# Kernel tuning notes

Measured on AMD Instinct MI355X. Metric: run time of the kernel, lower is better.

## Reference

```python
import jax, jax.numpy as jnp
import numpy as np

NUM_HEADS = 16
NUM_KV_HEADS = 4
ROPE_THETA = 10000.0


def apply_rope(x, position_ids, theta):
    # x: [B, S, h, d]; position_ids: [B, S]
    d = x.shape[-1]
    freqs = 1.0 / theta ** (jnp.arange(0, d, 2, dtype=jnp.float32) / d)  # [d/2]
    angles = position_ids.astype(jnp.float32)[..., None] * freqs          # [B, S, d/2]
    cos = jnp.cos(angles)[:, :, None, :]                                  # [B, S, 1, d/2]
    sin = jnp.sin(angles)[:, :, None, :]
    xr = x.astype(jnp.float32).reshape(*x.shape[:-1], d // 2, 2)
    x0, x1 = xr[..., 0], xr[..., 1]
    o0 = x0 * cos - x1 * sin
    o1 = x0 * sin + x1 * cos
    out = jnp.stack((o0, o1), axis=-1).reshape(*x.shape)
    return out.astype(x.dtype)


def setup_inputs() -> dict:
    key = jax.random.key(0)
    k0, k1, k2, k3, k4 = jax.random.split(key, 5)
    B, S, H = 1, 2048, 2048
    Hkv = H // (NUM_HEADS // NUM_KV_HEADS)  # 512
    init_scale = 0.02 / np.sqrt(H)
    return {
        "hidden_states": jax.random.normal(k0, (B, S, H), jnp.float32),
        "attention_mask": jnp.ones((B, S), jnp.int32),
        "segment_ids": jnp.zeros((B, S), jnp.int32),
        "position_ids": jnp.broadcast_to(jnp.arange(S, dtype=jnp.int32)[None], (B, S)),
        "Wq": jax.random.normal(k1, (H, H), jnp.float32) * init_scale,
        "Wk": jax.random.normal(k2, (H, Hkv), jnp.float32) * init_scale,
        "Wv": jax.random.normal(k3, (H, Hkv), jnp.float32) * init_scale,
        "Wo": jax.random.normal(k4, (H, H), jnp.float32) * init_scale,
    }


def reference(hidden_states, attention_mask, segment_ids, position_ids, Wq, Wk, Wv, Wo):
    B, S, H = hidden_states.shape
    nh, nkv = NUM_HEADS, NUM_KV_HEADS
    g = nh // nkv
    hd = H // nh

    xq = (hidden_states @ Wq).reshape(B, S, nh, hd)
    xk = (hidden_states @ Wk).reshape(B, S, nkv, hd)
    xv = (hidden_states @ Wv).reshape(B, S, nkv, hd)
    # GQA repeat: 'b s (h d) -> b s (h g) d' == repeat each kv head g times contiguously
    xk = jnp.repeat(xk, g, axis=2)  # [B, S, nh, hd]
    xv = jnp.repeat(xv, g, axis=2)

    xq = apply_rope(xq, position_ids, ROPE_THETA)
    xk = apply_rope(xk, position_ids, ROPE_THETA)

    # masks: causal AND padding AND segment
    causal = jnp.tril(jnp.ones((S, S), dtype=bool))[None, None]            # [1,1,S,S]
    pad = (attention_mask > 0)[:, None, None, :]                            # [B,1,1,S]
    seg = (segment_ids[:, :, None] == segment_ids[:, None, :])[:, None]     # [B,1,S,S]
    mask = causal & pad & seg                                               # [B,1,S,S]

    scale = 1.0 / np.sqrt(hd)
    logits = jnp.einsum("bqhd,bkhd->bhqk", xq.astype(jnp.float32), xk.astype(jnp.float32)) * scale
    logits = jnp.where(mask, logits, jnp.finfo(jnp.float32).min)
    probs = jax.nn.softmax(logits, axis=-1).astype(xv.dtype)
    attn = jnp.einsum("bhqk,bkhd->bqhd", probs, xv)                         # [B,S,nh,hd]

    out = attn.reshape(B, S, H) @ Wo
    return out
```

## Files before the change

kernel.cpp:

```cpp
#include <hip/hip_runtime.h>
#include <hip/hip_bf16.h>
#include <stdint.h>
#include <math.h>

#define SS 2048
#define HH 2048
#define NH 16
#define NKV 4
#define HD 128
#define HKV 512
#define NQKV 3072

typedef __bf16 bf16x8 __attribute__((ext_vector_type(8)));
typedef float f32x4 __attribute__((ext_vector_type(4)));

static_assert(sizeof(bf16x8) == 16, "bf16x8 must be 16B");

__device__ __forceinline__ void async_ld16(const void* gp, void* lp) {
  __builtin_amdgcn_global_load_lds(
      (const __attribute__((address_space(1))) unsigned int*)(uintptr_t)gp,
      (__attribute__((address_space(3))) unsigned int*)(uintptr_t)lp,
      16, 0, 0);
}

__device__ __forceinline__ unsigned short f2bu(float f) {
  __hip_bfloat16 b = __float2bfloat16(f);
  return *reinterpret_cast<unsigned short*>(&b);
}

__global__ __launch_bounds__(256) void k_prep1(
    const float* __restrict__ X, const float* __restrict__ Wq, const float* __restrict__ Wk,
    const float* __restrict__ Wv, const float* __restrict__ Wo,
    const int* __restrict__ amv, const int* __restrict__ seg, int* __restrict__ kseg,
    __hip_bfloat16* __restrict__ Xb, __hip_bfloat16* __restrict__ WqT,
    __hip_bfloat16* __restrict__ WkT, __hip_bfloat16* __restrict__ WvT,
    __hip_bfloat16* __restrict__ WoT) {
  __shared__ float tile[32][33];
  int b = blockIdx.x;
  if (b < 4096) {
    int i = b * 256 + threadIdx.y * 32 + threadIdx.x;
    float4 v = ((const float4*)X)[i];
    ushort4 o;
    o.x = f2bu(v.x); o.y = f2bu(v.y); o.z = f2bu(v.z); o.w = f2bu(v.w);
    ((ushort4*)Xb)[i] = o;
    return;
  }
  b -= 4096;
  if (b >= 10240) {
    int i = (b - 10240) * 256 + threadIdx.y * 32 + threadIdx.x;
    kseg[i] = (amv[i] > 0) ? seg[i] : 0x7fffffff;
    return;
  }
  const float* src; __hip_bfloat16* dst; int xtiles;
  if (b < 4096)      { src = Wq; dst = WqT; xtiles = 64; }
  else if (b < 8192) { src = Wo; dst = WoT; xtiles = 64; b -= 4096; }
  else if (b < 9216) { src = Wk; dst = WkT; xtiles = 16; b -= 8192; }
  else               { src = Wv; dst = WvT; xtiles = 16; b -= 9216; }
  const int C = xtiles * 32;
  int bx = (b % xtiles) * 32;
  int by = (b / xtiles) * 32;
  int tx = threadIdx.x, ty = threadIdx.y;
#pragma unroll
  for (int i = 0; i < 4; i++)
    tile[ty + i * 8][tx] = src[(size_t)(by + ty + i * 8) * C + bx + tx];
  __syncthreads();
#pragma unroll
  for (int i = 0; i < 4; i++)
    dst[(size_t)(bx + ty + i * 8) * HH + by + tx] = __float2bfloat16(tile[tx][ty + i * 8]);
}

__global__ __launch_bounds__(256, 3) void k_gemm_qkv(
    const __hip_bfloat16* __restrict__ A, const __hip_bfloat16* __restrict__ B,
    __hip_bfloat16* __restrict__ Qb, __hip_bfloat16* __restrict__ Kb,
    __hip_bfloat16* __restrict__ Vt, const int* __restrict__ pos) {
  __shared__ __align__(16) __hip_bfloat16 sA0[64 * 64];
  __shared__ __align__(16) __hip_bfloat16 sB0[128 * 64];
  __shared__ __align__(16) __hip_bfloat16 sA1[64 * 64];
  __shared__ __align__(16) __hip_bfloat16 sB1[128 * 64];
  const int tid = threadIdx.x;
  const int lane = tid & 63;
  const int wave = tid >> 6;
  const int bm = blockIdx.y * 64;
  const int bn = blockIdx.x * 128;
  const int wm = (wave & 1) * 32;
  const int wn = (wave >> 1) * 64;
  const int am = lane & 15;
  const int ch = lane >> 4;

  f32x4 acc[2][4] = {};

  auto stage = [&](__hip_bfloat16* sA, __hip_bfloat16* sB, int k0) {
#pragma unroll
    for (int q = 0; q < 2; q++) {
      int c = q * 256 + tid;
      int row = c >> 3, kp = c & 7;
      int col = (kp ^ (row & 7)) * 8;
      async_ld16(A + (size_t)(bm + row) * HH + k0 + col, (char*)sA + c * 16);
    }
#pragma unroll
    for (int q = 0; q < 4; q++) {
      int c = q * 256 + tid;
      int row = c >> 3, kp = c & 7;
      int col = (kp ^ (row & 7)) * 8;
      async_ld16(B + (size_t)(bn + row) * HH + k0 + col, (char*)sB + c * 16);
    }
  };
  auto compute = [&](const __hip_bfloat16* sA, const __hip_bfloat16* sB) {
#pragma unroll
    for (int kb = 0; kb < 2; kb++) {
      bf16x8 a[2], b[4];
#pragma unroll
      for (int i = 0; i < 2; i++) {
        int row = wm + i * 16 + am;
        a[i] = *(const bf16x8*)(sA + row * 64 + (((kb * 4 + ch) ^ (row & 7)) * 8));
      }
#pragma unroll
      for (int j = 0; j < 4; j++) {
        int row = wn + j * 16 + am;
        b[j] = *(const bf16x8*)(sB + row * 64 + (((kb * 4 + ch) ^ (row & 7)) * 8));
      }
#pragma unroll
      for (int i = 0; i < 2; i++)
#pragma unroll
        for (int j = 0; j < 4; j++)
          acc[i][j] = __builtin_amdgcn_mfma_f32_16x16x32_bf16(a[i], b[j], acc[i][j], 0, 0, 0);
    }
  };

  stage(sA0, sB0, 0);
  int k0 = 0;
  while (true) {
    __syncthreads();
    if (k0 + 64 < HH) stage(sA1, sB1, k0 + 64);
    compute(sA0, sB0);
    k0 += 64; if (k0 >= HH) break;
    __syncthreads();
    if (k0 + 64 < HH) stage(sA0, sB0, k0 + 64);
    compute(sA1, sB1);
    k0 += 64; if (k0 >= HH) break;
  }

  const bool isV = (bn >= HH + HKV);
  if (isV) {
#pragma unroll
    for (int j = 0; j < 4; j++) {
      int lc = bn + wn + j * 16 + am - (HH + HKV);
#pragma unroll
      for (int i = 0; i < 2; i++) {
        int row = bm + wm + i * 16 + ch * 4;
        ushort4 o;
        o.x = f2bu(acc[i][j][0]); o.y = f2bu(acc[i][j][1]);
        o.z = f2bu(acc[i][j][2]); o.w = f2bu(acc[i][j][3]);
        *(ushort4*)(Vt + (size_t)lc * SS + row) = o;
      }
    }
  } else {
    const float SCLQ = 0.08838834764831845f * 1.4426950408889634f;
    const float L2T_D64 = 0.20762050593046837f;
    const bool isQ = (bn < HH);
    float posr[2][4];
#pragma unroll
    for (int i = 0; i < 2; i++)
#pragma unroll
      for (int r = 0; r < 4; r++)
        posr[i][r] = (float)pos[bm + wm + i * 16 + ch * 4 + r];
    const float sgn = (am & 1) ? 1.0f : -1.0f;
#pragma unroll
    for (int j = 0; j < 4; j++) {
      int col = bn + wn + j * 16 + am;
      int lc = isQ ? col : (col - HH);
      float freq = exp2f(-L2T_D64 * (float)((lc >> 1) & 63));
#pragma unroll
      for (int i = 0; i < 2; i++)
#pragma unroll
        for (int r = 0; r < 4; r++) {
          float v = acc[i][j][r];
          float px = __shfl_xor(v, 1, 64);
          float ang = posr[i][r] * freq;
          float sn, cs;
          sincosf(ang, &sn, &cs);
          float o = v * cs + sgn * px * sn;
          int row = bm + wm + i * 16 + ch * 4 + r;
          if (isQ) Qb[(size_t)row * HH + col] = __float2bfloat16(o * SCLQ);
          else     Kb[(size_t)row * HKV + lc] = __float2bfloat16(o);
        }
    }
  }
}

__global__ __launch_bounds__(256, 3) void k_gemm_out(
    const __hip_bfloat16* __restrict__ A, const __hip_bfloat16* __restrict__ B,
    float* __restrict__ C) {
  __shared__ __align__(16) __hip_bfloat16 sA0[64 * 64];
  __shared__ __align__(16) __hip_bfloat16 sB0[128 * 64];
  __shared__ __align__(16) __hip_bfloat16 sA1[64 * 64];
  __shared__ __align__(16) __hip_bfloat16 sB1[128 * 64];
  const int tid = threadIdx.x;
  const int lane = tid & 63;
  const int wave = tid >> 6;
  const int bm = blockIdx.y * 64;
  const int bn = blockIdx.x * 128;
  const int wm = (wave & 1) * 32;
  const int wn = (wave >> 1) * 64;
  const int am = lane & 15;
  const int ch = lane >> 4;

  f32x4 acc[2][4] = {};

  auto stage = [&](__hip_bfloat16* sA, __hip_bfloat16* sB, int k0) {
#pragma unroll
    for (int q = 0; q < 2; q++) {
      int c = q * 256 + tid;
      int row = c >> 3, kp = c & 7;
      int col = (kp ^ (row & 7)) * 8;
      async_ld16(A + (size_t)(bm + row) * HH + k0 + col, (char*)sA + c * 16);
    }
#pragma unroll
    for (int q = 0; q < 4; q++) {
      int c = q * 256 + tid;
      int row = c >> 3, kp = c & 7;
      int col = (kp ^ (row & 7)) * 8;
      async_ld16(B + (size_t)(bn + row) * HH + k0 + col, (char*)sB + c * 16);
    }
  };
  auto compute = [&](const __hip_bfloat16* sA, const __hip_bfloat16* sB) {
#pragma unroll
    for (int kb = 0; kb < 2; kb++) {
      bf16x8 a[2], b[4];
#pragma unroll
      for (int i = 0; i < 2; i++) {
        int row = wm + i * 16 + am;
        a[i] = *(const bf16x8*)(sA + row * 64 + (((kb * 4 + ch) ^ (row & 7)) * 8));
      }
#pragma unroll
      for (int j = 0; j < 4; j++) {
        int row = wn + j * 16 + am;
        b[j] = *(const bf16x8*)(sB + row * 64 + (((kb * 4 + ch) ^ (row & 7)) * 8));
      }
#pragma unroll
      for (int i = 0; i < 2; i++)
#pragma unroll
        for (int j = 0; j < 4; j++)
          acc[i][j] = __builtin_amdgcn_mfma_f32_16x16x32_bf16(a[i], b[j], acc[i][j], 0, 0, 0);
    }
  };

  stage(sA0, sB0, 0);
  int k0 = 0;
  while (true) {
    __syncthreads();
    if (k0 + 64 < HH) stage(sA1, sB1, k0 + 64);
    compute(sA0, sB0);
    k0 += 64; if (k0 >= HH) break;
    __syncthreads();
    if (k0 + 64 < HH) stage(sA0, sB0, k0 + 64);
    compute(sA1, sB1);
    k0 += 64; if (k0 >= HH) break;
  }

#pragma unroll
  for (int i = 0; i < 2; i++)
#pragma unroll
    for (int j = 0; j < 4; j++)
#pragma unroll
      for (int r = 0; r < 4; r++) {
        int row = bm + wm + i * 16 + ch * 4 + r;
        int col = bn + wn + j * 16 + am;
        C[(size_t)row * HH + col] = acc[i][j][r];
      }
}

__global__ __launch_bounds__(512, 4) void k_attn(
    const __hip_bfloat16* __restrict__ Qb,
    const __hip_bfloat16* __restrict__ Kb,
    const __hip_bfloat16* __restrict__ Vt,
    const int* __restrict__ seg,
    const int* __restrict__ kseg,
    float* __restrict__ Obuf,
    float* __restrict__ Lbuf) {
  __shared__ __align__(16) __hip_bfloat16 sK[2][64 * 128];
  __shared__ __align__(16) __hip_bfloat16 sV[2][128 * 64];
  __shared__ __align__(16) __hip_bfloat16 sPall[8][16 * 64];

  const int bid = blockIdx.x;
  const int g = bid >> 5;
  const int qt = (bid < 256) ? (15 - g) : (g - 8);
  const int h = (bid >> 1) & 15;
  const int half = bid & 1;
  const int n0 = qt + 1;
  const int kt0 = half ? n0 : 0;
  const int kt1 = half ? (2 * qt + 2) : n0;

  const int kvh = h >> 2;
  const int tid = threadIdx.x, lane = tid & 63, w = tid >> 6;
  const int am = lane & 15, ch = lane >> 4;
  const int qrow0 = qt * 128 + w * 16;
  char* sP = (char*)&sPall[w][0];

  bf16x8 qf[4];
#pragma unroll
  for (int ks = 0; ks < 4; ks++)
    qf[ks] = *(const bf16x8*)(Qb + (size_t)(qrow0 + am) * HH + h * HD + ks * 32 + ch * 8);

  int segq[4];
#pragma unroll
  for (int r = 0; r < 4; r++) segq[r] = seg[qrow0 + ch * 4 + r];
  const int q0 = seg[qt * 128 + w * 16];
  const bool quni = __all((segq[0] == q0) && (segq[1] == q0) &&
                          (segq[2] == q0) && (segq[3] == q0));

  f32x4 o_acc[8] = {};
  float l_s[4] = {0.f, 0.f, 0.f, 0.f};

  auto stage = [&](int kt, int p) {
#pragma unroll
    for (int q = 0; q < 2; q++) {
      int c = q * 512 + tid;
      int row = c >> 4, kp = c & 15;
      int col = (kp ^ (row & 15)) * 8;
      async_ld16(Kb + (size_t)(kt * 64 + row) * HKV + kvh * 128 + col, (char*)sK[p] + c * 16);
    }
#pragma unroll
    for (int q = 0; q < 2; q++) {
      int c = q * 512 + tid;
      int row = c >> 3, kp = c & 7;
      int col = (kp ^ (row & 7)) * 8;
      async_ld16(Vt + (size_t)(kvh * 128 + row) * SS + kt * 64 + col, (char*)sV[p] + c * 16);
    }
  };

  stage(kt0, 0);
  for (int kt = kt0; kt < kt1; kt++) {
    const int p = (kt - kt0) & 1;
    const int kbase = kt * 64;
    const bool skip = (kbase > qrow0 + 15);
    __syncthreads();

    int kinfo[4];
    if (!skip) {
#pragma unroll
      for (int jt = 0; jt < 4; jt++) kinfo[jt] = kseg[kbase + jt * 16 + am];
    }
    if (kt + 1 < kt1) stage(kt + 1, p ^ 1);
    if (!skip) {
      f32x4 sacc[4] = {};
      __builtin_amdgcn_s_setprio(1);
#pragma unroll
      for (int ks = 0; ks < 4; ks++)
#pragma unroll
        for (int jt = 0; jt < 4; jt++) {
          bf16x8 kf = *(const bf16x8*)(sK[p] + (jt * 16 + am) * 128 + (((ks * 4 + ch) ^ am) * 8));
          sacc[jt] = __builtin_amdgcn_mfma_f32_16x16x32_bf16(qf[ks], kf, sacc[jt], 0, 0, 0);
        }
      __builtin_amdgcn_s_setprio(0);

      const bool needc = (kbase + 63 > qrow0);
      const bool fast = quni && !needc &&
          __all((kinfo[0] == q0) && (kinfo[1] == q0) &&
                (kinfo[2] == q0) && (kinfo[3] == q0));

      if (fast) {
#pragma unroll
        for (int jt = 0; jt < 4; jt++)
#pragma unroll
          for (int r = 0; r < 4; r++) {
            float pv = exp2f(sacc[jt][r] - 8.0f);
            l_s[r] += pv;
            int row = ch * 4 + r;
            int chunk = (jt * 2 + (am >> 3)) ^ (row & 7);
            *(__hip_bfloat16*)(sP + row * 128 + chunk * 16 + (am & 7) * 2) =
                __float2bfloat16(pv);
          }
      } else {
#pragma unroll
        for (int jt = 0; jt < 4; jt++) {
          int kk = kbase + jt * 16 + am;
#pragma unroll
          for (int r = 0; r < 4; r++) {
            int qrow = qrow0 + ch * 4 + r;
            bool ok = (kinfo[jt] == segq[r]) && (kk <= qrow);
            float pv = ok ? exp2f(sacc[jt][r] - 8.0f) : 0.0f;
            l_s[r] += pv;
            int row = ch * 4 + r;
            int chunk = (jt * 2 + (am >> 3)) ^ (row & 7);
            *(__hip_bfloat16*)(sP + row * 128 + chunk * 16 + (am & 7) * 2) =
                __float2bfloat16(pv);
          }
        }
      }

      __builtin_amdgcn_s_setprio(1);
#pragma unroll
      for (int ks = 0; ks < 2; ks++) {
        bf16x8 pf = *(const bf16x8*)(sP + am * 128 + (((ks * 4 + ch) ^ (am & 7)) * 16));
#pragma unroll
        for (int jt = 0; jt < 8; jt++) {
          int vrow = jt * 16 + am;
          bf16x8 vf = *(const bf16x8*)(sV[p] + vrow * 64 + (((ks * 4 + ch) ^ (vrow & 7)) * 8));
          o_acc[jt] = __builtin_amdgcn_mfma_f32_16x16x32_bf16(pf, vf, o_acc[jt], 0, 0, 0);
        }
      }
      __builtin_amdgcn_s_setprio(0);
    }
  }

#pragma unroll
  for (int off = 1; off < 16; off <<= 1)
#pragma unroll
    for (int r = 0; r < 4; r++) l_s[r] += __shfl_xor(l_s[r], off, 64);
  if (am == 0)
#pragma unroll
    for (int r = 0; r < 4; r++)
      unsafeAtomicAdd(Lbuf + (size_t)(qrow0 + ch * 4 + r) * NH + h, l_s[r]);
#pragma unroll
  for (int jt = 0; jt < 8; jt++)
#pragma unroll
    for (int r = 0; r < 4; r++) {
      int row = qrow0 + ch * 4 + r;
      unsafeAtomicAdd(Obuf + (size_t)row * HH + h * HD + jt * 16 + am, o_acc[jt][r]);
    }
}

__global__ __launch_bounds__(256) void k_norm(
    const float* __restrict__ Obuf, const float* __restrict__ Lbuf,
    __hip_bfloat16* __restrict__ Ab) {
  int i = blockIdx.x * 256 + threadIdx.x;
  int s = i >> 9;
  int hIdx = (i & 511) >> 5;
  float inv = 1.0f / Lbuf[(size_t)s * NH + hIdx];
  float4 v = ((const float4*)Obuf)[i];
  ushort4 o;
  o.x = f2bu(v.x * inv); o.y = f2bu(v.y * inv);
  o.z = f2bu(v.z * inv); o.w = f2bu(v.w * inv);
  ((ushort4*)Ab)[i] = o;
}

extern "C" void kernel_launch(void* const* d_in, const int* in_sizes, int n_in,
                              void* d_out, int out_size, void* d_ws, size_t ws_size,
                              hipStream_t stream) {
  const float* X  = (const float*)d_in[0];
  const int* amv  = (const int*)d_in[1];
  const int* seg  = (const int*)d_in[2];
  const int* pos  = (const int*)d_in[3];
  const float* Wq = (const float*)d_in[4];
  const float* Wk = (const float*)d_in[5];
  const float* Wv = (const float*)d_in[6];
  const float* Wo = (const float*)d_in[7];
  float* out = (float*)d_out;

  char* ws = (char*)d_ws;
  size_t off = 0;
  auto alloc = [&](size_t bytes) { void* p = ws + off; off += (bytes + 255) & ~(size_t)255; return p; };
  __hip_bfloat16* Xb   = (__hip_bfloat16*)alloc((size_t)SS * HH * 2);
  __hip_bfloat16* WqT  = (__hip_bfloat16*)alloc((size_t)HH * HH * 2);
  __hip_bfloat16* WkT  = (__hip_bfloat16*)alloc((size_t)HKV * HH * 2);
  __hip_bfloat16* WvT  = (__hip_bfloat16*)alloc((size_t)HKV * HH * 2);
  __hip_bfloat16* WoT  = (__hip_bfloat16*)alloc((size_t)HH * HH * 2);
  __hip_bfloat16* Qb   = (__hip_bfloat16*)alloc((size_t)SS * HH * 2);
  __hip_bfloat16* Kb   = (__hip_bfloat16*)alloc((size_t)SS * HKV * 2);
  __hip_bfloat16* Vt   = (__hip_bfloat16*)alloc((size_t)HKV * SS * 2);
  __hip_bfloat16* Ab   = (__hip_bfloat16*)alloc((size_t)SS * HH * 2);
  float*          Obuf = (float*)alloc((size_t)SS * HH * 4);
  float*          Lbuf = (float*)alloc((size_t)SS * NH * 4);
  int*            kseg = (int*)alloc((size_t)SS * 4);
  (void)WkT; (void)WvT;

  hipMemsetAsync(Obuf, 0, (size_t)SS * HH * 4 + ((size_t)SS * NH * 4 + 255 & ~(size_t)255), stream);
  k_prep1<<<dim3(14344), dim3(32, 8), 0, stream>>>(X, Wq, Wk, Wv, Wo, amv, seg, kseg,
                                                   Xb, WqT, WkT, WvT, WoT);
  k_gemm_qkv<<<dim3(NQKV / 128, SS / 64), 256, 0, stream>>>(Xb, WqT, Qb, Kb, Vt, pos);
  k_attn<<<dim3(512), dim3(512), 0, stream>>>(Qb, Kb, Vt, seg, kseg, Obuf, Lbuf);
  k_norm<<<dim3(SS * HH / 4 / 256), 256, 0, stream>>>(Obuf, Lbuf, Ab);
  k_gemm_out<<<dim3(HH / 128, SS / 64), 256, 0, stream>>>(Ab, WoT, out);
}
```

Before: 233.6 us.

## Triple-buffer GEMM K-loop with vmcnt waits and precompute RoPE sin/cos table

Both GEMM kernels move from a double-buffered loop with full __syncthreads to a three-stage LDS ring. Each step waits only on the oldest outstanding async loads (vmcnt(6)) before the barrier, so two stages of global-to-LDS loads stay in flight. This raises LDS use per block, and launch bounds drop from 3 to 2 blocks per CU. Separately, RoPE sin/cos values are precomputed into a 2048x64 table in the prep kernel and gathered in the QKV epilogue, replacing per-element sincosf. The table is indexed by the runtime position values, which it assumes fall below 2048.

```diff
diff --git a/kernel.cpp b/kernel.cpp
--- a/kernel.cpp
+++ b/kernel.cpp
@@ -32,6 +32,7 @@
     const float* __restrict__ X, const float* __restrict__ Wq, const float* __restrict__ Wk,
     const float* __restrict__ Wv, const float* __restrict__ Wo,
     const int* __restrict__ amv, const int* __restrict__ seg, int* __restrict__ kseg,
+    float2* __restrict__ rtab,
     __hip_bfloat16* __restrict__ Xb, __hip_bfloat16* __restrict__ WqT,
     __hip_bfloat16* __restrict__ WkT, __hip_bfloat16* __restrict__ WvT,
     __hip_bfloat16* __restrict__ WoT) {
@@ -46,6 +47,16 @@
     return;
   }
   b -= 4096;
+  if (b >= 10248) {
+    int i = (b - 10248) * 256 + threadIdx.y * 32 + threadIdx.x;
+    int p = i >> 6, f = i & 63;
+    const float L2T_D64 = 0.20762050593046837f;
+    float freq = exp2f(-L2T_D64 * (float)f);
+    float sn, cs;
+    sincosf((float)p * freq, &sn, &cs);
+    rtab[i] = make_float2(sn, cs);
+    return;
+  }
   if (b >= 10240) {
     int i = (b - 10240) * 256 + threadIdx.y * 32 + threadIdx.x;
     kseg[i] = (amv[i] > 0) ? seg[i] : 0x7fffffff;
@@ -69,14 +80,17 @@
     dst[(size_t)(bx + ty + i * 8) * HH + by + tx] = __float2bfloat16(tile[tx][ty + i * 8]);
 }
 
-__global__ __launch_bounds__(256, 3) void k_gemm_qkv(
+__global__ __launch_bounds__(256, 2) void k_gemm_qkv(
     const __hip_bfloat16* __restrict__ A, const __hip_bfloat16* __restrict__ B,
     __hip_bfloat16* __restrict__ Qb, __hip_bfloat16* __restrict__ Kb,
-    __hip_bfloat16* __restrict__ Vt, const int* __restrict__ pos) {
+    __hip_bfloat16* __restrict__ Vt, const int* __restrict__ pos,
+    const float2* __restrict__ rtab) {
   __shared__ __align__(16) __hip_bfloat16 sA0[64 * 64];
+  __shared__ __align__(16) __hip_bfloat16 sA1[64 * 64];
+  __shared__ __align__(16) __hip_bfloat16 sA2[64 * 64];
   __shared__ __align__(16) __hip_bfloat16 sB0[128 * 64];
-  __shared__ __align__(16) __hip_bfloat16 sA1[64 * 64];
   __shared__ __align__(16) __hip_bfloat16 sB1[128 * 64];
+  __shared__ __align__(16) __hip_bfloat16 sB2[128 * 64];
   const int tid = threadIdx.x;
   const int lane = tid & 63;
   const int wave = tid >> 6;
@@ -127,17 +141,19 @@
     }
   };
 
-  stage(sA0, sB0, 0);
-  int k0 = 0;
-  while (true) {
-    __syncthreads();
-    if (k0 + 64 < HH) stage(sA1, sB1, k0 + 64);
-    compute(sA0, sB0);
-    k0 += 64; if (k0 >= HH) break;
-    __syncthreads();
-    if (k0 + 64 < HH) stage(sA0, sB0, k0 + 64);
-    compute(sA1, sB1);
-    k0 += 64; if (k0 >= HH) break;
+  __hip_bfloat16 *cA = sA0, *nA = sA1, *fA = sA2;
+  __hip_bfloat16 *cB = sB0, *nB = sB1, *fB = sB2;
+  stage(cA, cB, 0);
+  stage(nA, nB, 64);
+  for (int t = 0; t < 32; ++t) {
+    if (t + 1 < 32) asm volatile("s_waitcnt vmcnt(6)" ::: "memory");
+    else            asm volatile("s_waitcnt vmcnt(0)" ::: "memory");
+    asm volatile("s_barrier" ::: "memory");
+    if (t + 2 < 32) stage(fA, fB, (t + 2) * 64);
+    compute(cA, cB);
+    __hip_bfloat16* tp;
+    tp = cA; cA = nA; nA = fA; fA = tp;
+    tp = cB; cB = nB; nB = fB; fB = tp;
   }
 
   const bool isV = (bn >= HH + HKV);
@@ -156,30 +172,27 @@
     }
   } else {
     const float SCLQ = 0.08838834764831845f * 1.4426950408889634f;
-    const float L2T_D64 = 0.20762050593046837f;
     const bool isQ = (bn < HH);
-    float posr[2][4];
+    int pint[2][4];
 #pragma unroll
     for (int i = 0; i < 2; i++)
 #pragma unroll
       for (int r = 0; r < 4; r++)
-        posr[i][r] = (float)pos[bm + wm + i * 16 + ch * 4 + r];
+        pint[i][r] = pos[bm + wm + i * 16 + ch * 4 + r];
     const float sgn = (am & 1) ? 1.0f : -1.0f;
 #pragma unroll
     for (int j = 0; j < 4; j++) {
       int col = bn + wn + j * 16 + am;
       int lc = isQ ? col : (col - HH);
-      float freq = exp2f(-L2T_D64 * (float)((lc >> 1) & 63));
+      int fidx = (lc >> 1) & 63;
 #pragma unroll
       for (int i = 0; i < 2; i++)
 #pragma unroll
         for (int r = 0; r < 4; r++) {
           float v = acc[i][j][r];
           float px = __shfl_xor(v, 1, 64);
-          float ang = posr[i][r] * freq;
-          float sn, cs;
-          sincosf(ang, &sn, &cs);
-          float o = v * cs + sgn * px * sn;
+          float2 sc = rtab[pint[i][r] * 64 + fidx];
+          float o = v * sc.y + sgn * px * sc.x;
           int row = bm + wm + i * 16 + ch * 4 + r;
           if (isQ) Qb[(size_t)row * HH + col] = __float2bfloat16(o * SCLQ);
           else     Kb[(size_t)row * HKV + lc] = __float2bfloat16(o);
@@ -188,13 +201,15 @@
   }
 }
 
-__global__ __launch_bounds__(256, 3) void k_gemm_out(
+__global__ __launch_bounds__(256, 2) void k_gemm_out(
     const __hip_bfloat16* __restrict__ A, const __hip_bfloat16* __restrict__ B,
     float* __restrict__ C) {
   __shared__ __align__(16) __hip_bfloat16 sA0[64 * 64];
+  __shared__ __align__(16) __hip_bfloat16 sA1[64 * 64];
+  __shared__ __align__(16) __hip_bfloat16 sA2[64 * 64];
   __shared__ __align__(16) __hip_bfloat16 sB0[128 * 64];
-  __shared__ __align__(16) __hip_bfloat16 sA1[64 * 64];
   __shared__ __align__(16) __hip_bfloat16 sB1[128 * 64];
+  __shared__ __align__(16) __hip_bfloat16 sB2[128 * 64];
   const int tid = threadIdx.x;
   const int lane = tid & 63;
   const int wave = tid >> 6;
@@ -245,17 +260,19 @@
     }
   };
 
-  stage(sA0, sB0, 0);
-  int k0 = 0;
-  while (true) {
-    __syncthreads();
-    if (k0 + 64 < HH) stage(sA1, sB1, k0 + 64);
-    compute(sA0, sB0);
-    k0 += 64; if (k0 >= HH) break;
-    __syncthreads();
-    if (k0 + 64 < HH) stage(sA0, sB0, k0 + 64);
-    compute(sA1, sB1);
-    k0 += 64; if (k0 >= HH) break;
+  __hip_bfloat16 *cA = sA0, *nA = sA1, *fA = sA2;
+  __hip_bfloat16 *cB = sB0, *nB = sB1, *fB = sB2;
+  stage(cA, cB, 0);
+  stage(nA, nB, 64);
+  for (int t = 0; t < 32; ++t) {
+    if (t + 1 < 32) asm volatile("s_waitcnt vmcnt(6)" ::: "memory");
+    else            asm volatile("s_waitcnt vmcnt(0)" ::: "memory");
+    asm volatile("s_barrier" ::: "memory");
+    if (t + 2 < 32) stage(fA, fB, (t + 2) * 64);
+    compute(cA, cB);
+    __hip_bfloat16* tp;
+    tp = cA; cA = nA; nA = fA; fA = tp;
+    tp = cB; cB = nB; nB = fB; fB = tp;
   }
 
 #pragma unroll
@@ -463,12 +480,13 @@
   float*          Obuf = (float*)alloc((size_t)SS * HH * 4);
   float*          Lbuf = (float*)alloc((size_t)SS * NH * 4);
   int*            kseg = (int*)alloc((size_t)SS * 4);
+  float2*         rtab = (float2*)alloc((size_t)SS * 64 * 8);
   (void)WkT; (void)WvT;
 
   hipMemsetAsync(Obuf, 0, (size_t)SS * HH * 4 + ((size_t)SS * NH * 4 + 255 & ~(size_t)255), stream);
-  k_prep1<<<dim3(14344), dim3(32, 8), 0, stream>>>(X, Wq, Wk, Wv, Wo, amv, seg, kseg,
+  k_prep1<<<dim3(14856), dim3(32, 8), 0, stream>>>(X, Wq, Wk, Wv, Wo, amv, seg, kseg, rtab,
                                                    Xb, WqT, WkT, WvT, WoT);
-  k_gemm_qkv<<<dim3(NQKV / 128, SS / 64), 256, 0, stream>>>(Xb, WqT, Qb, Kb, Vt, pos);
+  k_gemm_qkv<<<dim3(NQKV / 128, SS / 64), 256, 0, stream>>>(Xb, WqT, Qb, Kb, Vt, pos, rtab);
   k_attn<<<dim3(512), dim3(512), 0, stream>>>(Qb, Kb, Vt, seg, kseg, Obuf, Lbuf);
   k_norm<<<dim3(SS * HH / 4 / 256), 256, 0, stream>>>(Obuf, Lbuf, Ab);
   k_gemm_out<<<dim3(HH / 128, SS / 64), 256, 0, stream>>>(Ab, WoT, out);
```

Result: slower. 246.4 us (+5.5%).
